# Performance work log

Hardware: AMD Instinct MI355X
Metric: run time of the kernel (lower is better)

## Reference

```python
import jax, jax.numpy as jnp
import numpy as np

B, T, D = 1, 256, 80
CC = 256        # conv_channels
CCEP = 222      # ccep_size
K = 3           # kernel_size
FFT = 1024
HOP = 256
WIN = 512       # window_size = 2*hop
PF_K = 128      # ltv_postfilter_kernel_size


def conv1d_same(x, w, b, dilation=1):
    """x: (B, L, Cin), w: (Cout, Cin, K) -> (B, L, Cout), 'same' padding."""
    k = w.shape[-1]
    ke = (k - 1) * dilation + 1
    pad = ((ke - 1) // 2, ke - 1 - (ke - 1) // 2)
    y = jax.lax.conv_general_dilated(
        x, w, window_strides=(1,), padding=[pad], rhs_dilation=(dilation,),
        dimension_numbers=('NWC', 'OIW', 'NWC'))
    return y + b


def setup_inputs() -> dict:
    key = jax.random.key(0)
    ks = jax.random.split(key, 8)
    def mkw(k, o, i, kk, scale=1.0):
        return (jax.random.normal(k, (o, i, kk), jnp.float32) * scale / np.sqrt(i * kk)).astype(jnp.float32)
    x = jax.random.normal(ks[0], (B, T, D), jnp.float32)
    z = jax.random.normal(ks[1], (B, 1, T * HOP), jnp.float32)
    w1 = mkw(ks[2], CC, D, K);    b1 = jnp.zeros((CC,), jnp.float32)
    w2 = mkw(ks[3], CC, CC, K);   b2 = jnp.zeros((CC,), jnp.float32)
    w3 = mkw(ks[4], CCEP, CC, K, 0.1); b3 = jnp.zeros((CCEP,), jnp.float32)
    pf_w = mkw(ks[5], 1, 1, PF_K); pf_b = jnp.zeros((1,), jnp.float32)
    # quefrency norm buffer: cat(flip(1..111), 1..111)
    idx = jnp.arange(1, CCEP // 2 + 1, dtype=jnp.float32)
    quef_norm = jnp.concatenate([idx[::-1], idx])
    win = 0.5 * (1.0 - jnp.cos(2.0 * jnp.pi * jnp.arange(WIN, dtype=jnp.float32) / WIN))
    return dict(x=x, z=z, w1=w1, b1=b1, w2=w2, b2=b2, w3=w3, b3=b3,
                pf_w=pf_w, pf_b=pf_b, quef_norm=quef_norm, win=win)


def reference(x, z, w1, b1, w2, b2, w3, b3, pf_w, pf_b, quef_norm, win):
    # --- ConvLayers front-end: conv stack producing complex cepstrum per frame ---
    h = jax.nn.relu(conv1d_same(x, w1, b1))
    h = jax.nn.relu(conv1d_same(h, w2, b2))
    ccep = conv1d_same(h, w3, b3) / quef_norm           # (B, T, 222)
    # --- _ccep2impulse: pad -> FFT -> exp10(mag), keep phase -> IFFT.real ---
    pad = (FFT - CCEP) // 2
    cc = jnp.pad(ccep, ((0, 0), (0, 0), (pad, pad)))    # (B, T, 1024)
    Y = jnp.fft.fft(cc, n=FFT, axis=-1)
    mag = jnp.power(10.0, Y.real / 10.0)
    phase = Y.imag
    imp = jnp.fft.ifft(mag * jnp.cos(phase) + 1j * (mag * jnp.sin(phase)),
                       n=FFT, axis=-1).real.astype(jnp.float32)  # (B, T, 1024)
    # --- _conv_impulse: double unfold + per-frame matmul ---
    zp = jnp.pad(z, ((0, 0), (0, 0), (WIN // 2 - 1, WIN // 2)))      # (B,1,L+511)
    fidx = jnp.arange(T)[:, None] * HOP + jnp.arange(WIN)[None, :]   # (T, 512)
    frames = zp[:, :, fidx]                                          # (B,1,T,512)
    fp = jnp.pad(frames, ((0, 0), (0, 0), (0, 0), (FFT // 2 - 1, FFT // 2)))  # (B,1,T,1535)
    widx = jnp.arange(WIN)[:, None] + jnp.arange(FFT)[None, :]       # (512, 1024)
    wins = fp[:, :, :, widx]                                         # (B,1,T,512,1024)
    out = jnp.einsum('bctwk,btk->bctw', wins, imp)                   # (B,1,T,512)
    # --- _ola: window, split, roll-add, flatten ---
    out = out * win
    l, r = out[..., :HOP], out[..., HOP:]
    s = (l + jnp.roll(r, 1, axis=2)).reshape(B, 1, T * HOP)          # (B,1,L)
    # --- ltv postfilter: 1-ch conv1d (channels-last, 'same') ---
    y = conv1d_same(jnp.transpose(s, (0, 2, 1)), pf_w, pf_b)
    return jnp.transpose(y, (0, 2, 1))
```

## Files before the change

kernel.cpp:

```cpp
#include <hip/hip_runtime.h>

#define T_FRAMES 256
#define D_IN 80
#define CCH 256
#define CCEP 222
#define FFT_N 1024
#define HOP 256
#define WINL 512
#define PF_KT 128
#define ZLEN 65536

__device__ __forceinline__ unsigned br10(unsigned x) { return __brev(x) >> 22; }

__device__ __forceinline__ void conv_inner(const float4* __restrict__ wlds4,
                                           const float4* __restrict__ inlds4,
                                           int c, int fh, float* __restrict__ acc) {
  #pragma unroll
  for (int cg = 0; cg < 4; ++cg) {
    float4 w0 = wlds4[(cg * 3 + 0) * 256 + c];
    float4 w1v = wlds4[(cg * 3 + 1) * 256 + c];
    float4 w2v = wlds4[(cg * 3 + 2) * 256 + c];
    float4 xr[10];
    #pragma unroll
    for (int r = 0; r < 10; ++r) xr[r] = inlds4[(fh * 8 + r) * 4 + cg];
    #pragma unroll
    for (int j = 0; j < 8; ++j) {
      float4 xa = xr[j], xb = xr[j + 1], xc = xr[j + 2];
      acc[j] += xa.x * w0.x  + xb.x * w0.y  + xc.x * w0.z
              + xa.y * w0.w  + xb.y * w1v.x + xc.y * w1v.y
              + xa.z * w1v.z + xb.z * w1v.w + xc.z * w2v.x
              + xa.w * w2v.y + xb.w * w2v.z + xc.w * w2v.w;
    }
  }
}

__global__ __launch_bounds__(512) void conv1_k(const float* __restrict__ x, const float* __restrict__ w1,
                                               float* __restrict__ h1p) {
  __shared__ float4 wlds4[12 * 256];
  __shared__ float4 inlds4[18 * 4];
  const int kc = blockIdx.x, g = blockIdx.y, tid = threadIdx.x;
  const int t0 = g << 4;
  const float4* w14 = (const float4*)w1;
  const float4* x4 = (const float4*)x;
  #pragma unroll
  for (int it = 0; it < 6; ++it) {
    int idx = it * 512 + tid, cc = idx & 255, j4 = idx >> 8;
    wlds4[j4 * 256 + cc] = w14[cc * 60 + kc * 12 + j4];
  }
  if (tid < 72) {
    int r = tid >> 2, cg = tid & 3, tt = t0 - 1 + r;
    inlds4[tid] = (tt >= 0 && tt < T_FRAMES) ? x4[tt * 20 + kc * 4 + cg] : make_float4(0.f, 0.f, 0.f, 0.f);
  }
  __syncthreads();
  const int c = tid & 255, fh = tid >> 8;
  float acc[8] = {0.f, 0.f, 0.f, 0.f, 0.f, 0.f, 0.f, 0.f};
  conv_inner(wlds4, inlds4, c, fh, acc);
  const int ob = kc << 8;
  #pragma unroll
  for (int j = 0; j < 8; ++j) h1p[(ob + t0 + fh * 8 + j) * CCH + c] = acc[j];
}

__global__ __launch_bounds__(512) void conv2_k(const float* __restrict__ h1p, const float* __restrict__ b1,
                                               const float* __restrict__ w2, float* __restrict__ h2p) {
  __shared__ float4 wlds4[12 * 256];
  __shared__ float4 inlds4[18 * 4];
  const int kc = blockIdx.x, g = blockIdx.y, tid = threadIdx.x;
  const int t0 = g << 4;
  const float4* w24 = (const float4*)w2;
  const float4* h1p4 = (const float4*)h1p;
  const float4* b14 = (const float4*)b1;
  #pragma unroll
  for (int it = 0; it < 6; ++it) {
    int idx = it * 512 + tid, cc = idx & 255, j4 = idx >> 8;
    wlds4[j4 * 256 + cc] = w24[cc * 192 + kc * 12 + j4];
  }
  if (tid < 72) {
    int r = tid >> 2, cg = tid & 3, tt = t0 - 1 + r;
    float4 s = make_float4(0.f, 0.f, 0.f, 0.f);
    if (tt >= 0 && tt < T_FRAMES) {
      s = b14[kc * 4 + cg];
      #pragma unroll
      for (int p = 0; p < 5; ++p) {
        float4 v = h1p4[((p << 8) + tt) * 64 + kc * 4 + cg];
        s.x += v.x; s.y += v.y; s.z += v.z; s.w += v.w;
      }
      s.x = fmaxf(s.x, 0.f); s.y = fmaxf(s.y, 0.f); s.z = fmaxf(s.z, 0.f); s.w = fmaxf(s.w, 0.f);
    }
    inlds4[tid] = s;
  }
  __syncthreads();
  const int c = tid & 255, fh = tid >> 8;
  float acc[8] = {0.f, 0.f, 0.f, 0.f, 0.f, 0.f, 0.f, 0.f};
  conv_inner(wlds4, inlds4, c, fh, acc);
  const int ob = kc << 8;
  #pragma unroll
  for (int j = 0; j < 8; ++j) h2p[(ob + t0 + fh * 8 + j) * CCH + c] = acc[j];
}

__global__ __launch_bounds__(512) void conv3_k(const float* __restrict__ h2p, const float* __restrict__ b2,
                                               const float* __restrict__ w3, float* __restrict__ ccp) {
  __shared__ float4 wlds4[12 * 256];
  __shared__ float4 inlds4[18 * 4];
  const int kc = blockIdx.x, g = blockIdx.y, tid = threadIdx.x;
  const int t0 = g << 4;
  const float4* w34 = (const float4*)w3;
  const float4* h2p4 = (const float4*)h2p;
  const float4* b24 = (const float4*)b2;
  #pragma unroll
  for (int it = 0; it < 6; ++it) {
    int idx = it * 512 + tid, cc = idx & 255, j4 = idx >> 8;
    if (cc < CCEP) wlds4[j4 * 256 + cc] = w34[cc * 192 + kc * 12 + j4];
  }
  if (tid < 72) {
    int r = tid >> 2, cg = tid & 3, tt = t0 - 1 + r;
    float4 s = make_float4(0.f, 0.f, 0.f, 0.f);
    if (tt >= 0 && tt < T_FRAMES) {
      s = b24[kc * 4 + cg];
      #pragma unroll
      for (int p = 0; p < 16; ++p) {
        float4 v = h2p4[((p << 8) + tt) * 64 + kc * 4 + cg];
        s.x += v.x; s.y += v.y; s.z += v.z; s.w += v.w;
      }
      s.x = fmaxf(s.x, 0.f); s.y = fmaxf(s.y, 0.f); s.z = fmaxf(s.z, 0.f); s.w = fmaxf(s.w, 0.f);
    }
    inlds4[tid] = s;
  }
  __syncthreads();
  const int c = tid & 255, fh = tid >> 8;
  if (c < CCEP) {
    float acc[8] = {0.f, 0.f, 0.f, 0.f, 0.f, 0.f, 0.f, 0.f};
    conv_inner(wlds4, inlds4, c, fh, acc);
    const int ob = kc << 8;
    #pragma unroll
    for (int j = 0; j < 8; ++j) ccp[(ob + t0 + fh * 8 + j) * CCEP + c] = acc[j];
  }
}

__global__ __launch_bounds__(512) void fftltv_k(const float* __restrict__ ccp, const float* __restrict__ b3,
                                                const float* __restrict__ quef, const float* __restrict__ z,
                                                const float* __restrict__ win, float* __restrict__ outw) {
  __shared__ float2 U[FFT_N];
  int t = blockIdx.x, tid = threadIdx.x;
  for (int i = tid; i < FFT_N; i += 512) {
    unsigned q = br10((unsigned)i);
    float a = 0.f, bv = 0.f;
    if (q >= 401u && q < 623u) {
      int cq = (int)(q - 401u);
      float s = b3[cq];
      #pragma unroll
      for (int p = 0; p < 16; ++p) s += ccp[((p << 8) + t) * CCEP + cq];
      a = s / quef[cq];
    }
    if (q < 512u) {
      int idx = t * HOP + (int)q - 255;
      bv = (idx >= 0 && idx < ZLEN) ? z[idx] : 0.f;
    }
    U[i] = make_float2(a, bv);
  }
  __syncthreads();
  #pragma unroll
  for (int s = 1; s <= 10; ++s) {
    int half = 1 << (s - 1);
    int pos = tid & (half - 1);
    int i1 = ((tid >> (s - 1)) << s) + pos;
    int i2 = i1 + half;
    float ang = (-6.283185307179586f / (float)(1 << s)) * (float)pos;
    float sn, cs; __sincosf(ang, &sn, &cs);
    float2 v2 = U[i2], v1 = U[i1];
    float tr = cs * v2.x - sn * v2.y;
    float ti = cs * v2.y + sn * v2.x;
    U[i1] = make_float2(v1.x + tr, v1.y + ti);
    U[i2] = make_float2(v1.x - tr, v1.y - ti);
    __syncthreads();
  }
  {
    int j = tid;
    int mj = (FFT_N - j) & (FFT_N - 1);
    float2 Uj = U[j], Um = U[mj];
    float2 U5j = make_float2(0.f, 0.f);
    if (tid == 0) U5j = U[512];
    auto pcalc = [](float2 Uj, float2 Um) -> float2 {
      float Ar = 0.5f * (Uj.x + Um.x);
      float Ai = 0.5f * (Uj.y - Um.y);
      float Bx = 0.5f * (Uj.y + Um.y);
      float By = 0.5f * (Um.x - Uj.x);
      float mag = __expf(0.23025850929940457f * Ar);
      float sn, cs; __sincosf(Ai, &sn, &cs);
      float SPx = mag * cs, SPy = mag * sn;
      return make_float2(Bx * SPx + By * SPy, Bx * SPy - By * SPx);
    };
    float2 Pj = pcalc(Uj, Um);
    float2 P5 = (tid == 0) ? pcalc(U5j, U5j) : make_float2(0.f, 0.f);
    __syncthreads();
    U[j] = Pj;
    if (tid == 0) U[512] = P5;
    else U[mj] = make_float2(Pj.x, -Pj.y);
  }
  __syncthreads();
  #pragma unroll
  for (int s = 10; s >= 1; --s) {
    int half = 1 << (s - 1);
    int pos = tid & (half - 1);
    int i1 = ((tid >> (s - 1)) << s) + pos;
    int i2 = i1 + half;
    float ang = (6.283185307179586f / (float)(1 << s)) * (float)pos;
    float sn, cs; __sincosf(ang, &sn, &cs);
    float2 v1 = U[i1], v2 = U[i2];
    U[i1] = make_float2(v1.x + v2.x, v1.y + v2.y);
    float dr = v1.x - v2.x, di = v1.y - v2.y;
    U[i2] = make_float2(cs * dr - sn * di, cs * di + sn * dr);
    __syncthreads();
  }
  const float inv = 1.0f / (float)FFT_N;
  for (int i = tid; i < FFT_N; i += 512) {
    unsigned m = br10((unsigned)i);
    if (m < 512u) {
      int w = 511 - (int)m;
      outw[t * WINL + w] = U[i].x * inv * win[w];
    }
  }
}

__global__ __launch_bounds__(256) void pf_k(const float* __restrict__ outw, const float* __restrict__ pf_w,
                                            const float* __restrict__ pf_b, float* __restrict__ y) {
  __shared__ float sb[256 + PF_KT - 1];
  __shared__ float wpf[PF_KT];
  int n0 = blockIdx.x * 256;
  for (int i = threadIdx.x; i < 256 + PF_KT - 1; i += 256) {
    int m = n0 - 63 + i;
    float v = 0.f;
    if (m >= 0 && m < ZLEN) {
      int t = m >> 8, j = m & 255;
      v = outw[t * WINL + j] + outw[((t - 1) & 255) * WINL + HOP + j];
    }
    sb[i] = v;
  }
  if (threadIdx.x < PF_KT) wpf[threadIdx.x] = pf_w[threadIdx.x];
  __syncthreads();
  float acc = pf_b[0];
  #pragma unroll 8
  for (int j = 0; j < PF_KT; ++j) acc += sb[threadIdx.x + j] * wpf[j];
  y[n0 + threadIdx.x] = acc;
}

extern "C" void kernel_launch(void* const* d_in, const int* in_sizes, int n_in,
                              void* d_out, int out_size, void* d_ws, size_t ws_size,
                              hipStream_t stream) {
  const float* x    = (const float*)d_in[0];
  const float* z    = (const float*)d_in[1];
  const float* w1   = (const float*)d_in[2];
  const float* b1   = (const float*)d_in[3];
  const float* w2   = (const float*)d_in[4];
  const float* b2   = (const float*)d_in[5];
  const float* w3   = (const float*)d_in[6];
  const float* b3   = (const float*)d_in[7];
  const float* pf_w = (const float*)d_in[8];
  const float* pf_b = (const float*)d_in[9];
  const float* quef = (const float*)d_in[10];
  const float* win  = (const float*)d_in[11];
  float* out = (float*)d_out;
  float* ws  = (float*)d_ws;

  float* h1p  = ws;
  float* h2p  = h1p + 327680;
  float* ccp  = h2p + 1048576;
  float* outw = ccp + 909312;

  conv1_k<<<dim3(5, 16), 512, 0, stream>>>(x, w1, h1p);
  conv2_k<<<dim3(16, 16), 512, 0, stream>>>(h1p, b1, w2, h2p);
  conv3_k<<<dim3(16, 16), 512, 0, stream>>>(h2p, b2, w3, ccp);
  fftltv_k<<<T_FRAMES, 512, 0, stream>>>(ccp, b3, quef, z, win, outw);
  pf_k<<<ZLEN / 256, 256, 0, stream>>>(outw, pf_w, pf_b, out);
}
```

Before: 33.62 us.

## Transpose conv3 partial layout, parallelize partial-sum reduction, vectorize weight loads

Conv3 now writes its per-K-chunk partial sums with the chunk index innermost, so the FFT kernel can read the 16 partials for a channel as four contiguous float4 loads instead of 16 strided loads. Conv3's input reduction over 16 partials is spread across all 512 threads through a shared-memory staging buffer, replacing the 72-thread serial loop. Weight staging in all conv kernels is changed so each thread loads six consecutive float4s from one row. The trade-off is that conv3's output stores become strided scatters, and conv3 uses extra shared memory and an extra barrier.

New measurement: 39.90 us. 1.19x slower.

```diff
diff --git a/kernel.cpp b/kernel.cpp
--- a/kernel.cpp
+++ b/kernel.cpp
@@ -42,10 +42,11 @@
   const int t0 = g << 4;
   const float4* w14 = (const float4*)w1;
   const float4* x4 = (const float4*)x;
-  #pragma unroll
-  for (int it = 0; it < 6; ++it) {
-    int idx = it * 512 + tid, cc = idx & 255, j4 = idx >> 8;
-    wlds4[j4 * 256 + cc] = w14[cc * 60 + kc * 12 + j4];
+  {
+    const int row = tid & 255, seg = tid >> 8;
+    const float4* src = w14 + row * 60 + kc * 12 + seg * 6;
+    #pragma unroll
+    for (int m = 0; m < 6; ++m) wlds4[(seg * 6 + m) * 256 + row] = src[m];
   }
   if (tid < 72) {
     int r = tid >> 2, cg = tid & 3, tt = t0 - 1 + r;
@@ -69,10 +70,11 @@
   const float4* w24 = (const float4*)w2;
   const float4* h1p4 = (const float4*)h1p;
   const float4* b14 = (const float4*)b1;
-  #pragma unroll
-  for (int it = 0; it < 6; ++it) {
-    int idx = it * 512 + tid, cc = idx & 255, j4 = idx >> 8;
-    wlds4[j4 * 256 + cc] = w24[cc * 192 + kc * 12 + j4];
+  {
+    const int row = tid & 255, seg = tid >> 8;
+    const float4* src = w24 + row * 192 + kc * 12 + seg * 6;
+    #pragma unroll
+    for (int m = 0; m < 6; ++m) wlds4[(seg * 6 + m) * 256 + row] = src[m];
   }
   if (tid < 72) {
     int r = tid >> 2, cg = tid & 3, tt = t0 - 1 + r;
@@ -98,27 +100,55 @@
 }
 
 __global__ __launch_bounds__(512) void conv3_k(const float* __restrict__ h2p, const float* __restrict__ b2,
-                                               const float* __restrict__ w3, float* __restrict__ ccp) {
+                                               const float* __restrict__ w3, float* __restrict__ ccpt) {
   __shared__ float4 wlds4[12 * 256];
+  __shared__ float4 sred4[512 + 64];
   __shared__ float4 inlds4[18 * 4];
   const int kc = blockIdx.x, g = blockIdx.y, tid = threadIdx.x;
   const int t0 = g << 4;
   const float4* w34 = (const float4*)w3;
   const float4* h2p4 = (const float4*)h2p;
   const float4* b24 = (const float4*)b2;
-  #pragma unroll
-  for (int it = 0; it < 6; ++it) {
-    int idx = it * 512 + tid, cc = idx & 255, j4 = idx >> 8;
-    if (cc < CCEP) wlds4[j4 * 256 + cc] = w34[cc * 192 + kc * 12 + j4];
-  }
+  {
+    const int row = tid & 255, seg = tid >> 8;
+    if (row < CCEP) {
+      const float4* src = w34 + row * 192 + kc * 12 + seg * 6;
+      #pragma unroll
+      for (int m = 0; m < 6; ++m) wlds4[(seg * 6 + m) * 256 + row] = src[m];
+    }
+  }
+  {
+    int e = tid >> 3, pp = tid & 7;
+    int r = e >> 2, cg = e & 3, tt = t0 - 1 + r;
+    float4 v = make_float4(0.f, 0.f, 0.f, 0.f);
+    if (tt >= 0 && tt < T_FRAMES) {
+      float4 a = h2p4[((pp << 8) + tt) * 64 + kc * 4 + cg];
+      float4 b = h2p4[(((pp + 8) << 8) + tt) * 64 + kc * 4 + cg];
+      v = make_float4(a.x + b.x, a.y + b.y, a.z + b.z, a.w + b.w);
+    }
+    sred4[tid] = v;
+    if (tid < 64) {
+      int e2 = 64 + (tid >> 3), pp2 = tid & 7;
+      int r2 = e2 >> 2, cg2 = e2 & 3, tt2 = t0 - 1 + r2;
+      float4 v2 = make_float4(0.f, 0.f, 0.f, 0.f);
+      if (tt2 >= 0 && tt2 < T_FRAMES) {
+        float4 a = h2p4[((pp2 << 8) + tt2) * 64 + kc * 4 + cg2];
+        float4 b = h2p4[(((pp2 + 8) << 8) + tt2) * 64 + kc * 4 + cg2];
+        v2 = make_float4(a.x + b.x, a.y + b.y, a.z + b.z, a.w + b.w);
+      }
+      sred4[512 + tid] = v2;
+    }
+  }
+  __syncthreads();
   if (tid < 72) {
     int r = tid >> 2, cg = tid & 3, tt = t0 - 1 + r;
     float4 s = make_float4(0.f, 0.f, 0.f, 0.f);
     if (tt >= 0 && tt < T_FRAMES) {
       s = b24[kc * 4 + cg];
+      const float4* src = (tid < 64) ? &sred4[tid * 8] : &sred4[512 + (tid - 64) * 8];
       #pragma unroll
-      for (int p = 0; p < 16; ++p) {
-        float4 v = h2p4[((p << 8) + tt) * 64 + kc * 4 + cg];
+      for (int pp = 0; pp < 8; ++pp) {
+        float4 v = src[pp];
         s.x += v.x; s.y += v.y; s.z += v.z; s.w += v.w;
       }
       s.x = fmaxf(s.x, 0.f); s.y = fmaxf(s.y, 0.f); s.z = fmaxf(s.z, 0.f); s.w = fmaxf(s.w, 0.f);
@@ -130,13 +160,12 @@
   if (c < CCEP) {
     float acc[8] = {0.f, 0.f, 0.f, 0.f, 0.f, 0.f, 0.f, 0.f};
     conv_inner(wlds4, inlds4, c, fh, acc);
-    const int ob = kc << 8;
-    #pragma unroll
-    for (int j = 0; j < 8; ++j) ccp[(ob + t0 + fh * 8 + j) * CCEP + c] = acc[j];
-  }
-}
-
-__global__ __launch_bounds__(512) void fftltv_k(const float* __restrict__ ccp, const float* __restrict__ b3,
+    #pragma unroll
+    for (int j = 0; j < 8; ++j) ccpt[((t0 + fh * 8 + j) * CCEP + c) * 16 + kc] = acc[j];
+  }
+}
+
+__global__ __launch_bounds__(512) void fftltv_k(const float* __restrict__ ccpt, const float* __restrict__ b3,
                                                 const float* __restrict__ quef, const float* __restrict__ z,
                                                 const float* __restrict__ win, float* __restrict__ outw) {
   __shared__ float2 U[FFT_N];
@@ -146,9 +175,10 @@
     float a = 0.f, bv = 0.f;
     if (q >= 401u && q < 623u) {
       int cq = (int)(q - 401u);
-      float s = b3[cq];
-      #pragma unroll
-      for (int p = 0; p < 16; ++p) s += ccp[((p << 8) + t) * CCEP + cq];
+      const float4* c4 = (const float4*)(ccpt + ((size_t)t * CCEP + cq) * 16);
+      float4 s0 = c4[0], s1 = c4[1], s2 = c4[2], s3 = c4[3];
+      float s = b3[cq] + s0.x + s0.y + s0.z + s0.w + s1.x + s1.y + s1.z + s1.w
+                        + s2.x + s2.y + s2.z + s2.w + s3.x + s3.y + s3.z + s3.w;
       a = s / quef[cq];
     }
     if (q < 512u) {
@@ -263,12 +293,12 @@
 
   float* h1p  = ws;
   float* h2p  = h1p + 327680;
-  float* ccp  = h2p + 1048576;
-  float* outw = ccp + 909312;
+  float* ccpt = h2p + 1048576;
+  float* outw = ccpt + 909312;
 
   conv1_k<<<dim3(5, 16), 512, 0, stream>>>(x, w1, h1p);
   conv2_k<<<dim3(16, 16), 512, 0, stream>>>(h1p, b1, w2, h2p);
-  conv3_k<<<dim3(16, 16), 512, 0, stream>>>(h2p, b2, w3, ccp);
-  fftltv_k<<<T_FRAMES, 512, 0, stream>>>(ccp, b3, quef, z, win, outw);
+  conv3_k<<<dim3(16, 16), 512, 0, stream>>>(h2p, b2, w3, ccpt);
+  fftltv_k<<<T_FRAMES, 512, 0, stream>>>(ccpt, b3, quef, z, win, outw);
   pf_k<<<ZLEN / 256, 256, 0, stream>>>(outw, pf_w, pf_b, out);
 }
```

## Fuse conv1 into conv2 by recomputing layer-1 channel slice per block

Applied to the files above, without the earlier changes.

Merges the first and second conv kernels. Each conv2 block now recomputes the 16 layer-1 output channels it needs, for its 18-frame halo, directly from x and w1 held in shared memory. This drops one kernel launch and the h1p partial-sum round trip through global memory. In exchange, layer-1 work is recomputed redundantly across the 16 time-group blocks and the halo frames, and each block loads more into shared memory.

Result: no change. 33.04 us (-1.7%).

```diff
diff --git a/kernel.cpp b/kernel.cpp
--- a/kernel.cpp
+++ b/kernel.cpp
@@ -34,59 +34,46 @@
   }
 }
 
-__global__ __launch_bounds__(512) void conv1_k(const float* __restrict__ x, const float* __restrict__ w1,
-                                               float* __restrict__ h1p) {
+__global__ __launch_bounds__(512) void conv12_k(const float* __restrict__ x, const float* __restrict__ w1,
+                                                const float* __restrict__ b1, const float* __restrict__ w2,
+                                                float* __restrict__ h2p) {
   __shared__ float4 wlds4[12 * 256];
-  __shared__ float4 inlds4[18 * 4];
-  const int kc = blockIdx.x, g = blockIdx.y, tid = threadIdx.x;
-  const int t0 = g << 4;
-  const float4* w14 = (const float4*)w1;
-  const float4* x4 = (const float4*)x;
-  #pragma unroll
-  for (int it = 0; it < 6; ++it) {
-    int idx = it * 512 + tid, cc = idx & 255, j4 = idx >> 8;
-    wlds4[j4 * 256 + cc] = w14[cc * 60 + kc * 12 + j4];
-  }
-  if (tid < 72) {
-    int r = tid >> 2, cg = tid & 3, tt = t0 - 1 + r;
-    inlds4[tid] = (tt >= 0 && tt < T_FRAMES) ? x4[tt * 20 + kc * 4 + cg] : make_float4(0.f, 0.f, 0.f, 0.f);
-  }
-  __syncthreads();
-  const int c = tid & 255, fh = tid >> 8;
-  float acc[8] = {0.f, 0.f, 0.f, 0.f, 0.f, 0.f, 0.f, 0.f};
-  conv_inner(wlds4, inlds4, c, fh, acc);
-  const int ob = kc << 8;
-  #pragma unroll
-  for (int j = 0; j < 8; ++j) h1p[(ob + t0 + fh * 8 + j) * CCH + c] = acc[j];
-}
-
-__global__ __launch_bounds__(512) void conv2_k(const float* __restrict__ h1p, const float* __restrict__ b1,
-                                               const float* __restrict__ w2, float* __restrict__ h2p) {
-  __shared__ float4 wlds4[12 * 256];
+  __shared__ float  w1lds[240 * 16];
+  __shared__ float4 xlds4[20 * 20];
   __shared__ float4 inlds4[18 * 4];
   const int kc = blockIdx.x, g = blockIdx.y, tid = threadIdx.x;
   const int t0 = g << 4;
   const float4* w24 = (const float4*)w2;
-  const float4* h1p4 = (const float4*)h1p;
-  const float4* b14 = (const float4*)b1;
+  const float4* x4 = (const float4*)x;
   #pragma unroll
   for (int it = 0; it < 6; ++it) {
     int idx = it * 512 + tid, cc = idx & 255, j4 = idx >> 8;
     wlds4[j4 * 256 + cc] = w24[cc * 192 + kc * 12 + j4];
   }
-  if (tid < 72) {
-    int r = tid >> 2, cg = tid & 3, tt = t0 - 1 + r;
-    float4 s = make_float4(0.f, 0.f, 0.f, 0.f);
-    if (tt >= 0 && tt < T_FRAMES) {
-      s = b14[kc * 4 + cg];
-      #pragma unroll
-      for (int p = 0; p < 5; ++p) {
-        float4 v = h1p4[((p << 8) + tt) * 64 + kc * 4 + cg];
-        s.x += v.x; s.y += v.y; s.z += v.z; s.w += v.w;
-      }
-      s.x = fmaxf(s.x, 0.f); s.y = fmaxf(s.y, 0.f); s.z = fmaxf(s.z, 0.f); s.w = fmaxf(s.w, 0.f);
-    }
-    inlds4[tid] = s;
+  for (int idx = tid; idx < 3840; idx += 512) {
+    int ch = idx & 15, j = idx >> 4;
+    w1lds[j * 16 + ch] = w1[(kc * 16 + ch) * 240 + j];
+  }
+  if (tid < 400) {
+    int f = tid / 20, cg = tid - f * 20;
+    int tt = t0 - 2 + f;
+    xlds4[f * 20 + cg] = (tt >= 0 && tt < T_FRAMES) ? x4[tt * 20 + cg] : make_float4(0.f, 0.f, 0.f, 0.f);
+  }
+  __syncthreads();
+  if (tid < 288) {
+    int f = tid >> 4, ch = tid & 15;
+    int tt = t0 - 1 + f;
+    float acc = b1[kc * 16 + ch];
+    const float* x0 = (const float*)&xlds4[(f + 0) * 20];
+    const float* x1 = (const float*)&xlds4[(f + 1) * 20];
+    const float* x2 = (const float*)&xlds4[(f + 2) * 20];
+    #pragma unroll 8
+    for (int cin = 0; cin < D_IN; ++cin) {
+      acc += x0[cin] * w1lds[(cin * 3 + 0) * 16 + ch]
+           + x1[cin] * w1lds[(cin * 3 + 1) * 16 + ch]
+           + x2[cin] * w1lds[(cin * 3 + 2) * 16 + ch];
+    }
+    ((float*)inlds4)[f * 16 + ch] = (tt >= 0 && tt < T_FRAMES) ? fmaxf(acc, 0.f) : 0.f;
   }
   __syncthreads();
   const int c = tid & 255, fh = tid >> 8;
@@ -261,13 +248,11 @@
   float* out = (float*)d_out;
   float* ws  = (float*)d_ws;
 
-  float* h1p  = ws;
-  float* h2p  = h1p + 327680;
+  float* h2p  = ws;
   float* ccp  = h2p + 1048576;
   float* outw = ccp + 909312;
 
-  conv1_k<<<dim3(5, 16), 512, 0, stream>>>(x, w1, h1p);
-  conv2_k<<<dim3(16, 16), 512, 0, stream>>>(h1p, b1, w2, h2p);
+  conv12_k<<<dim3(16, 16), 512, 0, stream>>>(x, w1, b1, w2, h2p);
   conv3_k<<<dim3(16, 16), 512, 0, stream>>>(h2p, b2, w3, ccp);
   fftltv_k<<<T_FRAMES, 512, 0, stream>>>(ccp, b3, quef, z, win, outw);
   pf_k<<<ZLEN / 256, 256, 0, stream>>>(outw, pf_w, pf_b, out);
```
